# Kernel optimization log

Measured on AMD Instinct MI355X. Metric: run time of the kernel, lower is better.

The kernel has to match this reference:

```python
import jax, jax.numpy as jnp
import numpy as np

DIM = 1024
HEADS = 16
DIM_HEAD = 64
INNER = HEADS * DIM_HEAD
SCALE = DIM_HEAD ** -0.5


def setup_inputs() -> dict:
    key = jax.random.key(0)
    ks = jax.random.split(key, 7)
    B, S = 2, 2048
    x = jax.random.normal(ks[0], (B, S, DIM), dtype=jnp.float32)
    mask = jax.random.bernoulli(ks[1], 0.9, (B, S, S))  # bool [B,Q,K]
    init = lambda k, shape: jax.random.normal(k, shape, dtype=jnp.float32) * (shape[0] ** -0.5)
    Wq = init(ks[2], (DIM, INNER))
    Wk = init(ks[3], (DIM, INNER))
    Wv = init(ks[4], (DIM, INNER))
    Wo = init(ks[5], (INNER, DIM))
    bo = jnp.zeros((DIM,), dtype=jnp.float32)
    return {"x": x, "mask": mask, "Wq": Wq, "Wk": Wk, "Wv": Wv, "Wo": Wo, "bo": bo}


def reference(x, mask, Wq, Wk, Wv, Wo, bo):
    B, S, _ = x.shape
    # projections -> [B, H, S, Dh]
    q = (x @ Wq).reshape(B, S, HEADS, DIM_HEAD).transpose(0, 2, 1, 3)
    k = (x @ Wk).reshape(B, S, HEADS, DIM_HEAD).transpose(0, 2, 1, 3)
    v = (x @ Wv).reshape(B, S, HEADS, DIM_HEAD).transpose(0, 2, 1, 3)
    sim = jnp.einsum('bhid,bhjd->bhij', q, k) * SCALE
    attn_mask = mask[:, None]  # [B,1,Q,K]
    neg = -jnp.finfo(sim.dtype).max
    sim = jnp.where(attn_mask, sim, neg)
    attn = jax.nn.softmax(sim, axis=-1)
    # post-hoc mask renormalization
    attn = attn * attn_mask.astype(attn.dtype)
    attn = attn / jnp.maximum(attn.sum(axis=-1, keepdims=True), 1e-9)
    out = jnp.einsum('bhij,bhjd->bhid', attn, v)
    out = out.transpose(0, 2, 1, 3).reshape(B, S, INNER)
    return out @ Wo + bo
```

## Files before the change

### kernel.cpp

```cpp
#include <hip/hip_runtime.h>
#include <stdint.h>

#define SEQ 2048
#define DM 1024
#define NHEAD 16
#define HD 64

typedef __attribute__((ext_vector_type(8))) __bf16 bf16x8;
typedef __attribute__((ext_vector_type(4))) __bf16 bf16x4;
typedef __attribute__((ext_vector_type(4))) float f32x4;
typedef __attribute__((ext_vector_type(4))) short s16x4;
typedef __attribute__((ext_vector_type(4))) unsigned short u16x4;
typedef __attribute__((ext_vector_type(8))) unsigned short u16x8;
typedef __attribute__((ext_vector_type(4))) unsigned int u32x4;
typedef __attribute__((ext_vector_type(2))) unsigned int u32x2;

__device__ __forceinline__ unsigned short f2b(float f) {
  unsigned u = __builtin_bit_cast(unsigned, f);
  return (unsigned short)((u + 0x7FFFu + ((u >> 16) & 1u)) >> 16);
}

__device__ __forceinline__ float exp2_raw(float x) {
#if __has_builtin(__builtin_amdgcn_exp2f)
  return __builtin_amdgcn_exp2f(x);
#else
  float r;
  asm("v_exp_f32 %0, %1" : "=v"(r) : "v"(x));
  return r;
#endif
}

__device__ __forceinline__ void gload16(const void* g, void* l) {
  __builtin_amdgcn_global_load_lds((__attribute__((address_space(1))) void*)g,
                                   (__attribute__((address_space(3))) void*)l,
                                   16, 0, 0);
}

__global__ __launch_bounds__(256) void k_prep(const float* __restrict__ x,
                                              const float* __restrict__ W0,
                                              const float* __restrict__ W1,
                                              const float* __restrict__ W2,
                                              const float* __restrict__ W3,
                                              const void* __restrict__ maskp,
                                              unsigned short* __restrict__ xb,
                                              unsigned short* __restrict__ wt,
                                              unsigned* __restrict__ bits) {
  __shared__ float t[32][33];
  const unsigned blk = blockIdx.x;
  const int tid = threadIdx.x;

  if (blk < 1024) {
    const int lane = tid & 63;
    const int wv = blk * 4 + (tid >> 6);
    const unsigned* pw = (const unsigned*)maskp;
    unsigned s = pw[(size_t)wv * 512 + lane];
    unsigned long long ba = __ballot(s <= 1u);
    unsigned long long bf = __ballot(s == 0x3f800000u);
    bool dword = (bf != 0ull) || (ba == ~0ull);
    if (dword) {
      for (int gi = 0; gi < 32; ++gi) {
        unsigned d = pw[(size_t)wv * 2048 + gi * 64 + lane];
        unsigned long long bal = __ballot(d != 0u);
        if (lane == 0) bits[wv * 64 + gi * 2] = (unsigned)bal;
        if (lane == 32) bits[wv * 64 + gi * 2 + 1] = (unsigned)(bal >> 32);
      }
    } else {
      int wid = wv * 64 + lane;
      const u32x4* p = (const u32x4*)((const uint8_t*)maskp + (size_t)wid * 32);
      u32x4 v0 = p[0], v1 = p[1];
      unsigned word = 0;
      #pragma unroll
      for (int e = 0; e < 4; ++e) {
        unsigned d = v0[e];
        #pragma unroll
        for (int by = 0; by < 4; ++by)
          word |= (((d >> (8 * by)) & 0xffu) ? 1u : 0u) << (4 * e + by);
        d = v1[e];
        #pragma unroll
        for (int by = 0; by < 4; ++by)
          word |= (((d >> (8 * by)) & 0xffu) ? 1u : 0u) << (16 + 4 * e + by);
      }
      bits[wid] = word;
    }
  } else if (blk < 3072) {
    size_t i = (size_t)(blk - 1024) * 256 + tid;
    const f32x4* xv = (const f32x4*)x;
    f32x4 a = xv[i * 2], b = xv[i * 2 + 1];
    u16x8 o;
    o[0] = f2b(a[0]); o[1] = f2b(a[1]); o[2] = f2b(a[2]); o[3] = f2b(a[3]);
    o[4] = f2b(b[0]); o[5] = f2b(b[1]); o[6] = f2b(b[2]); o[7] = f2b(b[3]);
    ((u16x8*)xb)[i] = o;
  } else {
    unsigned idx = blk - 3072;
    int bx_ = idx & 31, by_ = (idx >> 5) & 31, z = idx >> 10;
    const float* W = (z == 0) ? W0 : (z == 1) ? W1 : (z == 2) ? W2 : W3;
    unsigned short* o = wt + (size_t)z * DM * DM;
    int r = tid >> 3, c4 = (tid & 7) << 2;
    f32x4 v = *(const f32x4*)&W[(size_t)(by_ * 32 + r) * DM + bx_ * 32 + c4];
    t[r][c4 + 0] = v[0]; t[r][c4 + 1] = v[1]; t[r][c4 + 2] = v[2]; t[r][c4 + 3] = v[3];
    __syncthreads();
    u16x4 ov;
    ov[0] = f2b(t[c4 + 0][r]); ov[1] = f2b(t[c4 + 1][r]);
    ov[2] = f2b(t[c4 + 2][r]); ov[3] = f2b(t[c4 + 3][r]);
    *(u16x4*)&o[(size_t)(bx_ * 32 + r) * DM + by_ * 32 + c4] = ov;
  }
}


#define BM 128
#define BN 128
#define BK 64

__device__ __forceinline__ void stage_tile64(const unsigned short* __restrict__ src,
                                             int row0, int kk, void* lds, int tid) {
  #pragma unroll
  for (int i = 0; i < 4; ++i) {
    int row = i * 32 + (tid >> 3);
    int cs = (tid & 7) ^ (row & 7);
    gload16(src + (size_t)(row0 + row) * DM + kk + cs * 8, (char*)lds + i * 4096 + tid * 16);
  }
}

__global__ __launch_bounds__(256) void k_gemm_qkv(const unsigned short* __restrict__ A,
                                                  const unsigned short* __restrict__ Wt,
                                                  unsigned short* __restrict__ Qb,
                                                  unsigned short* __restrict__ Kb,
                                                  unsigned short* __restrict__ Vt) {
  __shared__ __align__(16) unsigned short As[BM * BK];
  __shared__ __align__(16) unsigned short Bs[BN * BK];
  int z = blockIdx.y;
  const unsigned short* Bt = Wt + (size_t)z * DM * DM;
  int tid = threadIdx.x;
  int lane = tid & 63, w = tid >> 6;
  int li = lane & 15, g = lane >> 4;
  unsigned bx = blockIdx.x;
  unsigned sw = (bx & 7) * 32 + (bx >> 3);
  int bm = sw >> 3, bn = sw & 7;
  int row0 = bm * BM, col0 = bn * BN;
  int m0 = (w >> 1) * 64, n0 = (w & 1) * 64;
  f32x4 acc[4][4];
  #pragma unroll
  for (int i = 0; i < 4; ++i)
    #pragma unroll
    for (int j = 0; j < 4; ++j) acc[i][j] = (f32x4){0.f, 0.f, 0.f, 0.f};

  for (int kk = 0; kk < DM; kk += BK) {
    stage_tile64(A, row0, kk, As, tid);
    stage_tile64(Bt, col0, kk, Bs, tid);
    __syncthreads();
    #pragma unroll
    for (int kk2 = 0; kk2 < 2; ++kk2) {
      bf16x8 af[4], bfr[4];
      #pragma unroll
      for (int mi = 0; mi < 4; ++mi)
        af[mi] = *(const bf16x8*)((const char*)As + (m0 + mi * 16 + li) * 128 +
                                  (((kk2 * 4 + g) ^ (li & 7)) << 4));
      #pragma unroll
      for (int ni = 0; ni < 4; ++ni)
        bfr[ni] = *(const bf16x8*)((const char*)Bs + (n0 + ni * 16 + li) * 128 +
                                   (((kk2 * 4 + g) ^ (li & 7)) << 4));
      #pragma unroll
      for (int mi = 0; mi < 4; ++mi)
        #pragma unroll
        for (int ni = 0; ni < 4; ++ni)
          acc[mi][ni] = __builtin_amdgcn_mfma_f32_16x16x32_bf16(af[mi], bfr[ni], acc[mi][ni], 0, 0, 0);
    }
    __syncthreads();
  }

  if (z == 2) {
    #pragma unroll
    for (int mi = 0; mi < 4; ++mi)
      #pragma unroll
      for (int ni = 0; ni < 4; ++ni) {
        int mb = row0 + m0 + mi * 16 + g * 4;
        int n = col0 + n0 + ni * 16 + li;
        int bb = mb >> 11, s = mb & 2047;
        u16x4 ov;
        #pragma unroll
        for (int r = 0; r < 4; ++r) ov[r] = f2b(acc[mi][ni][r]);
        *(u16x4*)&Vt[((size_t)(bb * DM + n)) * SEQ + s] = ov;
      }
  } else {
    unsigned short* O = (z == 0) ? Qb : Kb;
    float sc = (z == 0) ? 0.18033688f : 1.0f;
    #pragma unroll
    for (int mi = 0; mi < 4; ++mi)
      #pragma unroll
      for (int ni = 0; ni < 4; ++ni) {
        int n = col0 + n0 + ni * 16 + li;
        #pragma unroll
        for (int r = 0; r < 4; ++r) {
          int m = row0 + m0 + mi * 16 + g * 4 + r;
          O[(size_t)m * DM + n] = f2b(acc[mi][ni][r] * sc);
        }
      }
  }
}

__global__ __launch_bounds__(256) void k_gemm_o(const unsigned short* __restrict__ A,
                                                const unsigned short* __restrict__ Bt,
                                                const float* __restrict__ bo,
                                                float* __restrict__ out) {
  __shared__ __align__(16) unsigned short As[BM * BK];
  __shared__ __align__(16) unsigned short Bs[BN * BK];
  int tid = threadIdx.x;
  int lane = tid & 63, w = tid >> 6;
  int li = lane & 15, g = lane >> 4;
  unsigned bx = blockIdx.x;
  unsigned sw = (bx & 7) * 32 + (bx >> 3);
  int bm = sw >> 3, bn = sw & 7;
  int row0 = bm * BM, col0 = bn * BN;
  int m0 = (w >> 1) * 64, n0 = (w & 1) * 64;
  f32x4 acc[4][4];
  #pragma unroll
  for (int i = 0; i < 4; ++i)
    #pragma unroll
    for (int j = 0; j < 4; ++j) acc[i][j] = (f32x4){0.f, 0.f, 0.f, 0.f};

  for (int kk = 0; kk < DM; kk += BK) {
    stage_tile64(A, row0, kk, As, tid);
    stage_tile64(Bt, col0, kk, Bs, tid);
    __syncthreads();
    #pragma unroll
    for (int kk2 = 0; kk2 < 2; ++kk2) {
      bf16x8 af[4], bfr[4];
      #pragma unroll
      for (int mi = 0; mi < 4; ++mi)
        af[mi] = *(const bf16x8*)((const char*)As + (m0 + mi * 16 + li) * 128 +
                                  (((kk2 * 4 + g) ^ (li & 7)) << 4));
      #pragma unroll
      for (int ni = 0; ni < 4; ++ni)
        bfr[ni] = *(const bf16x8*)((const char*)Bs + (n0 + ni * 16 + li) * 128 +
                                   (((kk2 * 4 + g) ^ (li & 7)) << 4));
      #pragma unroll
      for (int mi = 0; mi < 4; ++mi)
        #pragma unroll
        for (int ni = 0; ni < 4; ++ni)
          acc[mi][ni] = __builtin_amdgcn_mfma_f32_16x16x32_bf16(af[mi], bfr[ni], acc[mi][ni], 0, 0, 0);
    }
    __syncthreads();
  }

  #pragma unroll
  for (int mi = 0; mi < 4; ++mi)
    #pragma unroll
    for (int ni = 0; ni < 4; ++ni) {
      int n = col0 + n0 + ni * 16 + li;
      float bias = bo[n];
      #pragma unroll
      for (int r = 0; r < 4; ++r) {
        int m = row0 + m0 + mi * 16 + g * 4 + r;
        out[(size_t)m * DM + n] = acc[mi][ni][r] + bias;
      }
    }
}

__global__ __launch_bounds__(256) void k_attn(const unsigned short* __restrict__ Qm,
                                              const unsigned short* __restrict__ Km,
                                              const unsigned short* __restrict__ Vt,
                                              const unsigned* __restrict__ bits,
                                              unsigned short* __restrict__ AO) {
  __shared__ __align__(16) char kvbuf[2][16384];
  const int tid = threadIdx.x;
  const int lane = tid & 63;
  const int w = tid >> 6;
  const int li = lane & 15, g = lane >> 4;
  unsigned id = blockIdx.x;
  unsigned swz = (id & 7) * 64 + (id >> 3);
  const int qb = swz & 15;
  const int h = (swz >> 4) & 15;
  const int b = swz >> 8;
  const int q0 = qb * 128;
  const size_t qrow0w = (size_t)b * SEQ + q0 + w * 32;

  const char* Kg = (const char*)Km + ((size_t)b * SEQ * DM + h * HD) * 2;
  const char* Vg = (const char*)Vt + ((size_t)(b * DM + h * HD)) * SEQ * 2;

  auto stage = [&](int buf, int kb) {
    char* base = &kvbuf[buf][0];
    #pragma unroll
    for (int i = 0; i < 2; ++i) {
      int o = (w * 2 + i) * 1024 + lane * 16;
      int row = o >> 7, c = (o >> 4) & 7;
      int cs = (c ^ (row & 7)) << 4;
      gload16(Kg + (size_t)(kb + row) * 2048 + cs, base + o);
      gload16(Vg + (size_t)row * 4096 + (size_t)kb * 2 + cs, base + 8192 + o);
    }
  };

  bf16x8 qf[2][2];
  #pragma unroll
  for (int is = 0; is < 2; ++is)
    #pragma unroll
    for (int kc = 0; kc < 2; ++kc)
      qf[is][kc] = *(const bf16x8*)(Qm + (qrow0w + is * 16 + li) * DM + h * HD + kc * 32 + g * 8);

  f32x4 acc[2][4];
  f32x4 accl[2];
  #pragma unroll
  for (int is = 0; is < 2; ++is) {
    #pragma unroll
    for (int ds = 0; ds < 4; ++ds) acc[is][ds] = (f32x4){0.f, 0.f, 0.f, 0.f};
    accl[is] = (f32x4){0.f, 0.f, 0.f, 0.f};
  }
  bf16x4 onesb;
  onesb[0] = onesb[1] = onesb[2] = onesb[3] = (li == 0) ? (__bf16)1.0f : (__bf16)0.0f;
  const s16x4 ones = __builtin_bit_cast(s16x4, onesb);

  const unsigned* mr[2] = {bits + (qrow0w + li) * (SEQ / 32),
                           bits + (qrow0w + 16 + li) * (SEQ / 32)};
  const int sh0 = g * 4;

  stage(0, 0);
  __syncthreads();
  int cur = 0;

  for (int t = 0; t < SEQ / 64; ++t) {
    unsigned mw[2][2];
    #pragma unroll
    for (int is = 0; is < 2; ++is) {
      u32x2 mv = *(const u32x2*)(mr[is] + t * 2);
      mw[is][0] = mv[0];
      mw[is][1] = mv[1];
    }
    if (t + 1 < SEQ / 64) stage(cur ^ 1, (t + 1) * 64);

    const char* Kl = &kvbuf[cur][0];
    const char* Vl = &kvbuf[cur][8192];

    const f32x4 minit = (f32x4){-16.f, -16.f, -16.f, -16.f};
    f32x4 st[2][4];
    #pragma unroll
    for (int kt = 0; kt < 4; ++kt) {
      bf16x8 k0 = *(const bf16x8*)(Kl + (kt * 16 + li) * 128 + (((0 + g) ^ (li & 7)) << 4));
      bf16x8 k1 = *(const bf16x8*)(Kl + (kt * 16 + li) * 128 + (((4 + g) ^ (li & 7)) << 4));
      #pragma unroll
      for (int is = 0; is < 2; ++is) {
        st[is][kt] = __builtin_amdgcn_mfma_f32_16x16x32_bf16(k0, qf[is][0], minit, 0, 0, 0);
        st[is][kt] = __builtin_amdgcn_mfma_f32_16x16x32_bf16(k1, qf[is][1], st[is][kt], 0, 0, 0);
      }
    }

    s16x4 vf[4][4];
    #pragma unroll
    for (int ds = 0; ds < 4; ++ds)
      #pragma unroll
      for (int kt = 0; kt < 4; ++kt)
        vf[ds][kt] = *(const s16x4*)(Vl + (ds * 16 + li) * 128 +
                                     (((kt * 2 + (g >> 1)) ^ (li & 7)) << 4) + ((g & 1) << 3));

    #pragma unroll
    for (int is = 0; is < 2; ++is) {
      bf16x4 pb[4];
      #pragma unroll
      for (int kt = 0; kt < 4; ++kt) {
        unsigned mwv = mw[is][kt >> 1];
        #pragma unroll
        for (int r = 0; r < 4; ++r) {
          float ex = exp2_raw(st[is][kt][r]);
          int sext = __builtin_amdgcn_sbfe((int)mwv, (sh0 + (kt & 1) * 16 + r) & 31, 1);
          ex = __builtin_bit_cast(float, __builtin_bit_cast(int, ex) & sext);
          pb[kt][r] = (__bf16)ex;
        }
      }
      #pragma unroll
      for (int ds = 0; ds < 4; ++ds) {
        #pragma unroll
        for (int kt = 0; kt < 4; ++kt)
          acc[is][ds] = __builtin_amdgcn_mfma_f32_16x16x16bf16_1k(
              vf[ds][kt], __builtin_bit_cast(s16x4, pb[kt]), acc[is][ds], 0, 0, 0);
      }
      #pragma unroll
      for (int kt = 0; kt < 4; ++kt)
        accl[is] = __builtin_amdgcn_mfma_f32_16x16x16bf16_1k(
            ones, __builtin_bit_cast(s16x4, pb[kt]), accl[is], 0, 0, 0);
    }
    __syncthreads();
    cur ^= 1;
  }

  #pragma unroll
  for (int is = 0; is < 2; ++is) {
    float lv = __shfl(accl[is][0], li);
    float inv = 1.f / fmaxf(lv, 1e-9f);
    #pragma unroll
    for (int ds = 0; ds < 4; ++ds) {
      u16x4 ov;
      #pragma unroll
      for (int r = 0; r < 4; ++r) ov[r] = f2b(acc[is][ds][r] * inv);
      *(u16x4*)(AO + (qrow0w + is * 16 + li) * DM + h * HD + ds * 16 + g * 4) = ov;
    }
  }
}


extern "C" void kernel_launch(void* const* d_in, const int* in_sizes, int n_in,
                              void* d_out, int out_size, void* d_ws, size_t ws_size,
                              hipStream_t stream) {
  const float* x = (const float*)d_in[0];
  const void* mk = d_in[1];
  const float* Wq = (const float*)d_in[2];
  const float* Wk = (const float*)d_in[3];
  const float* Wv = (const float*)d_in[4];
  const float* Wo = (const float*)d_in[5];
  const float* bo = (const float*)d_in[6];
  float* out = (float*)d_out;
  char* ws = (char*)d_ws;

  unsigned short* xb = (unsigned short*)(ws);
  unsigned short* wt = (unsigned short*)(ws + ((size_t)8 << 20));
  unsigned short* Qb = (unsigned short*)(ws + ((size_t)16 << 20));
  unsigned short* Kb = (unsigned short*)(ws + ((size_t)24 << 20));
  unsigned short* Vt = (unsigned short*)(ws + ((size_t)32 << 20));
  unsigned* bits = (unsigned*)(ws + ((size_t)40 << 20));
  unsigned short* AO = xb;

  hipLaunchKernelGGL(k_prep, dim3(7168), dim3(256), 0, stream,
                     x, Wq, Wk, Wv, Wo, mk, xb, wt, bits);
  hipLaunchKernelGGL(k_gemm_qkv, dim3(256, 3), dim3(256), 0, stream, xb, wt, Qb, Kb, Vt);
  hipLaunchKernelGGL(k_attn, dim3(512), dim3(256), 0, stream, Qb, Kb, Vt, bits, AO);
  hipLaunchKernelGGL(k_gemm_o, dim3(256), dim3(256), 0, stream, AO, wt + (size_t)3 * DM * DM, bo, out);
}
```

Baseline: 137.3 us.

## Split attention block across 8 waves with 16 query rows each

The attention kernel now launches 512 threads (8 waves) per block instead of 4, and each wave handles 16 query rows instead of 32. K/V tile staging is spread over all 512 threads with one load each. This cuts per-wave register use and raises the number of waves available to hide latency. In exchange, each wave reuses every K/V LDS fragment across half as many query rows, so LDS reads per unit of MFMA work roughly double.

Result: no change. 136.3 us (-0.7%).

```diff
diff --git a/kernel.cpp b/kernel.cpp
--- a/kernel.cpp
+++ b/kernel.cpp
@@ -256,11 +256,11 @@
     }
 }
 
-__global__ __launch_bounds__(256) void k_attn(const unsigned short* __restrict__ Qm,
-                                              const unsigned short* __restrict__ Km,
-                                              const unsigned short* __restrict__ Vt,
-                                              const unsigned* __restrict__ bits,
-                                              unsigned short* __restrict__ AO) {
+__global__ __launch_bounds__(512, 4) void k_attn(const unsigned short* __restrict__ Qm,
+                                                 const unsigned short* __restrict__ Km,
+                                                 const unsigned short* __restrict__ Vt,
+                                                 const unsigned* __restrict__ bits,
+                                                 unsigned short* __restrict__ AO) {
   __shared__ __align__(16) char kvbuf[2][16384];
   const int tid = threadIdx.x;
   const int lane = tid & 63;
@@ -272,44 +272,34 @@
   const int h = (swz >> 4) & 15;
   const int b = swz >> 8;
   const int q0 = qb * 128;
-  const size_t qrow0w = (size_t)b * SEQ + q0 + w * 32;
+  const size_t qrow0w = (size_t)b * SEQ + q0 + w * 16;
 
   const char* Kg = (const char*)Km + ((size_t)b * SEQ * DM + h * HD) * 2;
   const char* Vg = (const char*)Vt + ((size_t)(b * DM + h * HD)) * SEQ * 2;
 
   auto stage = [&](int buf, int kb) {
     char* base = &kvbuf[buf][0];
-    #pragma unroll
-    for (int i = 0; i < 2; ++i) {
-      int o = (w * 2 + i) * 1024 + lane * 16;
-      int row = o >> 7, c = (o >> 4) & 7;
-      int cs = (c ^ (row & 7)) << 4;
-      gload16(Kg + (size_t)(kb + row) * 2048 + cs, base + o);
-      gload16(Vg + (size_t)row * 4096 + (size_t)kb * 2 + cs, base + 8192 + o);
-    }
+    int o = tid * 16;
+    int row = o >> 7, c = (o >> 4) & 7;
+    int cs = (c ^ (row & 7)) << 4;
+    gload16(Kg + (size_t)(kb + row) * 2048 + cs, base + o);
+    gload16(Vg + (size_t)row * 4096 + (size_t)kb * 2 + cs, base + 8192 + o);
   };
 
-  bf16x8 qf[2][2];
-  #pragma unroll
-  for (int is = 0; is < 2; ++is)
-    #pragma unroll
-    for (int kc = 0; kc < 2; ++kc)
-      qf[is][kc] = *(const bf16x8*)(Qm + (qrow0w + is * 16 + li) * DM + h * HD + kc * 32 + g * 8);
-
-  f32x4 acc[2][4];
-  f32x4 accl[2];
-  #pragma unroll
-  for (int is = 0; is < 2; ++is) {
-    #pragma unroll
-    for (int ds = 0; ds < 4; ++ds) acc[is][ds] = (f32x4){0.f, 0.f, 0.f, 0.f};
-    accl[is] = (f32x4){0.f, 0.f, 0.f, 0.f};
-  }
+  bf16x8 qf[2];
+  #pragma unroll
+  for (int kc = 0; kc < 2; ++kc)
+    qf[kc] = *(const bf16x8*)(Qm + (qrow0w + li) * DM + h * HD + kc * 32 + g * 8);
+
+  f32x4 acc[4];
+  f32x4 accl = (f32x4){0.f, 0.f, 0.f, 0.f};
+  #pragma unroll
+  for (int ds = 0; ds < 4; ++ds) acc[ds] = (f32x4){0.f, 0.f, 0.f, 0.f};
   bf16x4 onesb;
   onesb[0] = onesb[1] = onesb[2] = onesb[3] = (li == 0) ? (__bf16)1.0f : (__bf16)0.0f;
   const s16x4 ones = __builtin_bit_cast(s16x4, onesb);
 
-  const unsigned* mr[2] = {bits + (qrow0w + li) * (SEQ / 32),
-                           bits + (qrow0w + 16 + li) * (SEQ / 32)};
+  const unsigned* mr = bits + (qrow0w + li) * (SEQ / 32);
   const int sh0 = g * 4;
 
   stage(0, 0);
@@ -317,29 +307,20 @@
   int cur = 0;
 
   for (int t = 0; t < SEQ / 64; ++t) {
-    unsigned mw[2][2];
-    #pragma unroll
-    for (int is = 0; is < 2; ++is) {
-      u32x2 mv = *(const u32x2*)(mr[is] + t * 2);
-      mw[is][0] = mv[0];
-      mw[is][1] = mv[1];
-    }
+    u32x2 mv = *(const u32x2*)(mr + t * 2);
     if (t + 1 < SEQ / 64) stage(cur ^ 1, (t + 1) * 64);
 
     const char* Kl = &kvbuf[cur][0];
     const char* Vl = &kvbuf[cur][8192];
 
     const f32x4 minit = (f32x4){-16.f, -16.f, -16.f, -16.f};
-    f32x4 st[2][4];
+    f32x4 st[4];
     #pragma unroll
     for (int kt = 0; kt < 4; ++kt) {
       bf16x8 k0 = *(const bf16x8*)(Kl + (kt * 16 + li) * 128 + (((0 + g) ^ (li & 7)) << 4));
       bf16x8 k1 = *(const bf16x8*)(Kl + (kt * 16 + li) * 128 + (((4 + g) ^ (li & 7)) << 4));
-      #pragma unroll
-      for (int is = 0; is < 2; ++is) {
-        st[is][kt] = __builtin_amdgcn_mfma_f32_16x16x32_bf16(k0, qf[is][0], minit, 0, 0, 0);
-        st[is][kt] = __builtin_amdgcn_mfma_f32_16x16x32_bf16(k1, qf[is][1], st[is][kt], 0, 0, 0);
-      }
+      st[kt] = __builtin_amdgcn_mfma_f32_16x16x32_bf16(k0, qf[0], minit, 0, 0, 0);
+      st[kt] = __builtin_amdgcn_mfma_f32_16x16x32_bf16(k1, qf[1], st[kt], 0, 0, 0);
     }
 
     s16x4 vf[4][4];
@@ -350,47 +331,42 @@
         vf[ds][kt] = *(const s16x4*)(Vl + (ds * 16 + li) * 128 +
                                      (((kt * 2 + (g >> 1)) ^ (li & 7)) << 4) + ((g & 1) << 3));
 
-    #pragma unroll
-    for (int is = 0; is < 2; ++is) {
-      bf16x4 pb[4];
-      #pragma unroll
-      for (int kt = 0; kt < 4; ++kt) {
-        unsigned mwv = mw[is][kt >> 1];
-        #pragma unroll
-        for (int r = 0; r < 4; ++r) {
-          float ex = exp2_raw(st[is][kt][r]);
-          int sext = __builtin_amdgcn_sbfe((int)mwv, (sh0 + (kt & 1) * 16 + r) & 31, 1);
-          ex = __builtin_bit_cast(float, __builtin_bit_cast(int, ex) & sext);
-          pb[kt][r] = (__bf16)ex;
-        }
-      }
-      #pragma unroll
-      for (int ds = 0; ds < 4; ++ds) {
-        #pragma unroll
-        for (int kt = 0; kt < 4; ++kt)
-          acc[is][ds] = __builtin_amdgcn_mfma_f32_16x16x16bf16_1k(
-              vf[ds][kt], __builtin_bit_cast(s16x4, pb[kt]), acc[is][ds], 0, 0, 0);
-      }
+    bf16x4 pb[4];
+    #pragma unroll
+    for (int kt = 0; kt < 4; ++kt) {
+      unsigned mwv = mv[kt >> 1];
+      #pragma unroll
+      for (int r = 0; r < 4; ++r) {
+        float ex = exp2_raw(st[kt][r]);
+        int sext = __builtin_amdgcn_sbfe((int)mwv, (sh0 + (kt & 1) * 16 + r) & 31, 1);
+        ex = __builtin_bit_cast(float, __builtin_bit_cast(int, ex) & sext);
+        pb[kt][r] = (__bf16)ex;
+      }
+    }
+    #pragma unroll
+    for (int ds = 0; ds < 4; ++ds) {
       #pragma unroll
       for (int kt = 0; kt < 4; ++kt)
-        accl[is] = __builtin_amdgcn_mfma_f32_16x16x16bf16_1k(
-            ones, __builtin_bit_cast(s16x4, pb[kt]), accl[is], 0, 0, 0);
-    }
+        acc[ds] = __builtin_amdgcn_mfma_f32_16x16x16bf16_1k(
+            vf[ds][kt], __builtin_bit_cast(s16x4, pb[kt]), acc[ds], 0, 0, 0);
+    }
+    #pragma unroll
+    for (int kt = 0; kt < 4; ++kt)
+      accl = __builtin_amdgcn_mfma_f32_16x16x16bf16_1k(
+          ones, __builtin_bit_cast(s16x4, pb[kt]), accl, 0, 0, 0);
+
     __syncthreads();
     cur ^= 1;
   }
 
-  #pragma unroll
-  for (int is = 0; is < 2; ++is) {
-    float lv = __shfl(accl[is][0], li);
-    float inv = 1.f / fmaxf(lv, 1e-9f);
-    #pragma unroll
-    for (int ds = 0; ds < 4; ++ds) {
-      u16x4 ov;
-      #pragma unroll
-      for (int r = 0; r < 4; ++r) ov[r] = f2b(acc[is][ds][r] * inv);
-      *(u16x4*)(AO + (qrow0w + is * 16 + li) * DM + h * HD + ds * 16 + g * 4) = ov;
-    }
+  float lv = __shfl(accl[0], li);
+  float inv = 1.f / fmaxf(lv, 1e-9f);
+  #pragma unroll
+  for (int ds = 0; ds < 4; ++ds) {
+    u16x4 ov;
+    #pragma unroll
+    for (int r = 0; r < 4; ++r) ov[r] = f2b(acc[ds][r] * inv);
+    *(u16x4*)(AO + (qrow0w + li) * DM + h * HD + ds * 16 + g * 4) = ov;
   }
 }
 
@@ -419,6 +395,6 @@
   hipLaunchKernelGGL(k_prep, dim3(7168), dim3(256), 0, stream,
                      x, Wq, Wk, Wv, Wo, mk, xb, wt, bits);
   hipLaunchKernelGGL(k_gemm_qkv, dim3(256, 3), dim3(256), 0, stream, xb, wt, Qb, Kb, Vt);
-  hipLaunchKernelGGL(k_attn, dim3(512), dim3(256), 0, stream, Qb, Kb, Vt, bits, AO);
+  hipLaunchKernelGGL(k_attn, dim3(512), dim3(512), 0, stream, Qb, Kb, Vt, bits, AO);
   hipLaunchKernelGGL(k_gemm_o, dim3(256), dim3(256), 0, stream, AO, wt + (size_t)3 * DM * DM, bo, out);
 }
```

## Split attention key tiles across two waves per query group with LDS reduction

Applied to the files above, without the earlier changes.

The attention kernel doubles its block size to 512 threads. Pairs of waves now share the same 32 query rows, and each wave handles half of every 64-key tile. At the end, the partial PV accumulators and row sums are reduced through shared memory, reusing the K/V buffer. The aim is to raise wave-level parallelism and latency hiding on a grid of only 512 blocks, at the cost of an extra barrier, an LDS reduction, and Q fragments loaded redundantly by both waves of a pair.

After: 137.1 us. No clear change (-0.2%).

```diff
diff --git a/kernel.cpp b/kernel.cpp
--- a/kernel.cpp
+++ b/kernel.cpp
@@ -256,15 +256,18 @@
     }
 }
 
-__global__ __launch_bounds__(256) void k_attn(const unsigned short* __restrict__ Qm,
-                                              const unsigned short* __restrict__ Km,
-                                              const unsigned short* __restrict__ Vt,
-                                              const unsigned* __restrict__ bits,
-                                              unsigned short* __restrict__ AO) {
+__global__ __launch_bounds__(512, 4) void k_attn(const unsigned short* __restrict__ Qm,
+                                                 const unsigned short* __restrict__ Km,
+                                                 const unsigned short* __restrict__ Vt,
+                                                 const unsigned* __restrict__ bits,
+                                                 unsigned short* __restrict__ AO) {
   __shared__ __align__(16) char kvbuf[2][16384];
+  __shared__ float lbuf[4][64][2];
   const int tid = threadIdx.x;
   const int lane = tid & 63;
   const int w = tid >> 6;
+  const int qw = w >> 1;
+  const int kh = w & 1;
   const int li = lane & 15, g = lane >> 4;
   unsigned id = blockIdx.x;
   unsigned swz = (id & 7) * 64 + (id >> 3);
@@ -272,21 +275,18 @@
   const int h = (swz >> 4) & 15;
   const int b = swz >> 8;
   const int q0 = qb * 128;
-  const size_t qrow0w = (size_t)b * SEQ + q0 + w * 32;
+  const size_t qrow0w = (size_t)b * SEQ + q0 + qw * 32;
 
   const char* Kg = (const char*)Km + ((size_t)b * SEQ * DM + h * HD) * 2;
   const char* Vg = (const char*)Vt + ((size_t)(b * DM + h * HD)) * SEQ * 2;
 
   auto stage = [&](int buf, int kb) {
     char* base = &kvbuf[buf][0];
-    #pragma unroll
-    for (int i = 0; i < 2; ++i) {
-      int o = (w * 2 + i) * 1024 + lane * 16;
-      int row = o >> 7, c = (o >> 4) & 7;
-      int cs = (c ^ (row & 7)) << 4;
-      gload16(Kg + (size_t)(kb + row) * 2048 + cs, base + o);
-      gload16(Vg + (size_t)row * 4096 + (size_t)kb * 2 + cs, base + 8192 + o);
-    }
+    int o = tid * 16;
+    int row = o >> 7, c = (o >> 4) & 7;
+    int cs = (c ^ (row & 7)) << 4;
+    gload16(Kg + (size_t)(kb + row) * 2048 + cs, base + o);
+    gload16(Vg + (size_t)row * 4096 + (size_t)kb * 2 + cs, base + 8192 + o);
   };
 
   bf16x8 qf[2][2];
@@ -308,8 +308,8 @@
   onesb[0] = onesb[1] = onesb[2] = onesb[3] = (li == 0) ? (__bf16)1.0f : (__bf16)0.0f;
   const s16x4 ones = __builtin_bit_cast(s16x4, onesb);
 
-  const unsigned* mr[2] = {bits + (qrow0w + li) * (SEQ / 32),
-                           bits + (qrow0w + 16 + li) * (SEQ / 32)};
+  const unsigned* mr[2] = {bits + (qrow0w + li) * (SEQ / 32) + kh,
+                           bits + (qrow0w + 16 + li) * (SEQ / 32) + kh};
   const int sh0 = g * 4;
 
   stage(0, 0);
@@ -317,24 +317,19 @@
   int cur = 0;
 
   for (int t = 0; t < SEQ / 64; ++t) {
-    unsigned mw[2][2];
-    #pragma unroll
-    for (int is = 0; is < 2; ++is) {
-      u32x2 mv = *(const u32x2*)(mr[is] + t * 2);
-      mw[is][0] = mv[0];
-      mw[is][1] = mv[1];
-    }
+    unsigned mw[2] = {mr[0][t * 2], mr[1][t * 2]};
     if (t + 1 < SEQ / 64) stage(cur ^ 1, (t + 1) * 64);
 
     const char* Kl = &kvbuf[cur][0];
     const char* Vl = &kvbuf[cur][8192];
-
     const f32x4 minit = (f32x4){-16.f, -16.f, -16.f, -16.f};
-    f32x4 st[2][4];
-    #pragma unroll
-    for (int kt = 0; kt < 4; ++kt) {
-      bf16x8 k0 = *(const bf16x8*)(Kl + (kt * 16 + li) * 128 + (((0 + g) ^ (li & 7)) << 4));
-      bf16x8 k1 = *(const bf16x8*)(Kl + (kt * 16 + li) * 128 + (((4 + g) ^ (li & 7)) << 4));
+
+    f32x4 st[2][2];
+    #pragma unroll
+    for (int kt = 0; kt < 2; ++kt) {
+      int krow = kh * 32 + kt * 16 + li;
+      bf16x8 k0 = *(const bf16x8*)(Kl + krow * 128 + (((0 + g) ^ (li & 7)) << 4));
+      bf16x8 k1 = *(const bf16x8*)(Kl + krow * 128 + (((4 + g) ^ (li & 7)) << 4));
       #pragma unroll
       for (int is = 0; is < 2; ++is) {
         st[is][kt] = __builtin_amdgcn_mfma_f32_16x16x32_bf16(k0, qf[is][0], minit, 0, 0, 0);
@@ -342,24 +337,24 @@
       }
     }
 
-    s16x4 vf[4][4];
+    s16x4 vf[4][2];
     #pragma unroll
     for (int ds = 0; ds < 4; ++ds)
       #pragma unroll
-      for (int kt = 0; kt < 4; ++kt)
+      for (int kt = 0; kt < 2; ++kt)
         vf[ds][kt] = *(const s16x4*)(Vl + (ds * 16 + li) * 128 +
-                                     (((kt * 2 + (g >> 1)) ^ (li & 7)) << 4) + ((g & 1) << 3));
+                                     (((kh * 4 + kt * 2 + (g >> 1)) ^ (li & 7)) << 4) +
+                                     ((g & 1) << 3));
 
     #pragma unroll
     for (int is = 0; is < 2; ++is) {
-      bf16x4 pb[4];
-      #pragma unroll
-      for (int kt = 0; kt < 4; ++kt) {
-        unsigned mwv = mw[is][kt >> 1];
+      bf16x4 pb[2];
+      #pragma unroll
+      for (int kt = 0; kt < 2; ++kt) {
         #pragma unroll
         for (int r = 0; r < 4; ++r) {
           float ex = exp2_raw(st[is][kt][r]);
-          int sext = __builtin_amdgcn_sbfe((int)mwv, (sh0 + (kt & 1) * 16 + r) & 31, 1);
+          int sext = __builtin_amdgcn_sbfe((int)mw[is], (kt * 16 + sh0 + r) & 31, 1);
           ex = __builtin_bit_cast(float, __builtin_bit_cast(int, ex) & sext);
           pb[kt][r] = (__bf16)ex;
         }
@@ -367,12 +362,12 @@
       #pragma unroll
       for (int ds = 0; ds < 4; ++ds) {
         #pragma unroll
-        for (int kt = 0; kt < 4; ++kt)
+        for (int kt = 0; kt < 2; ++kt)
           acc[is][ds] = __builtin_amdgcn_mfma_f32_16x16x16bf16_1k(
               vf[ds][kt], __builtin_bit_cast(s16x4, pb[kt]), acc[is][ds], 0, 0, 0);
       }
       #pragma unroll
-      for (int kt = 0; kt < 4; ++kt)
+      for (int kt = 0; kt < 2; ++kt)
         accl[is] = __builtin_amdgcn_mfma_f32_16x16x16bf16_1k(
             ones, __builtin_bit_cast(s16x4, pb[kt]), accl[is], 0, 0, 0);
     }
@@ -380,16 +375,37 @@
     cur ^= 1;
   }
 
-  #pragma unroll
-  for (int is = 0; is < 2; ++is) {
-    float lv = __shfl(accl[is][0], li);
-    float inv = 1.f / fmaxf(lv, 1e-9f);
-    #pragma unroll
-    for (int ds = 0; ds < 4; ++ds) {
-      u16x4 ov;
-      #pragma unroll
-      for (int r = 0; r < 4; ++r) ov[r] = f2b(acc[is][ds][r] * inv);
-      *(u16x4*)(AO + (qrow0w + is * 16 + li) * DM + h * HD + ds * 16 + g * 4) = ov;
+  {
+    f32x4* scr = (f32x4*)&kvbuf[0][0] + (size_t)(qw * 64 + lane) * 8;
+    if (kh) {
+      #pragma unroll
+      for (int is = 0; is < 2; ++is)
+        #pragma unroll
+        for (int ds = 0; ds < 4; ++ds)
+          scr[(is * 4 + ds) ^ (lane & 7)] = acc[is][ds];
+      lbuf[qw][lane][0] = accl[0][0];
+      lbuf[qw][lane][1] = accl[1][0];
+    }
+    __syncthreads();
+    if (!kh) {
+      #pragma unroll
+      for (int is = 0; is < 2; ++is)
+        #pragma unroll
+        for (int ds = 0; ds < 4; ++ds)
+          acc[is][ds] += scr[(is * 4 + ds) ^ (lane & 7)];
+      float lsum[2] = {accl[0][0] + lbuf[qw][lane][0], accl[1][0] + lbuf[qw][lane][1]};
+      #pragma unroll
+      for (int is = 0; is < 2; ++is) {
+        float lv = __shfl(lsum[is], li);
+        float inv = 1.f / fmaxf(lv, 1e-9f);
+        #pragma unroll
+        for (int ds = 0; ds < 4; ++ds) {
+          u16x4 ov;
+          #pragma unroll
+          for (int r = 0; r < 4; ++r) ov[r] = f2b(acc[is][ds][r] * inv);
+          *(u16x4*)(AO + (qrow0w + is * 16 + li) * DM + h * HD + ds * 16 + g * 4) = ov;
+        }
+      }
     }
   }
 }
@@ -419,6 +435,6 @@
   hipLaunchKernelGGL(k_prep, dim3(7168), dim3(256), 0, stream,
                      x, Wq, Wk, Wv, Wo, mk, xb, wt, bits);
   hipLaunchKernelGGL(k_gemm_qkv, dim3(256, 3), dim3(256), 0, stream, xb, wt, Qb, Kb, Vt);
-  hipLaunchKernelGGL(k_attn, dim3(512), dim3(256), 0, stream, Qb, Kb, Vt, bits, AO);
+  hipLaunchKernelGGL(k_attn, dim3(512), dim3(512), 0, stream, Qb, Kb, Vt, bits, AO);
   hipLaunchKernelGGL(k_gemm_o, dim3(256), dim3(256), 0, stream, AO, wt + (size_t)3 * DM * DM, bo, out);
 }
```
